# Kernel tuning notes

Measured on AMD Instinct MI355X. Metric: run time of the kernel, lower is better.

Reference implementation:

```python
import jax, jax.numpy as jnp
import numpy as np

EPS = 1e-05


def setup_inputs() -> dict:
    key = jax.random.key(0)
    ks = jax.random.split(key, 6)
    B, L, D = 16, 4096, 1024
    x = jax.random.normal(ks[0], (B, L, D), dtype=jnp.float32)
    prev_count = jax.random.randint(ks[1], (B,), 1, 5).astype(jnp.int32)  # prior_count-like, >=1
    prev_mean = jnp.zeros((B, D), dtype=jnp.float32)   # prior_mean init = 0
    prev_var = jnp.ones((B, D), dtype=jnp.float32)     # exp(prior_logv) with logv init 0
    weight = 0.02 * jax.random.normal(ks[2], (D,), dtype=jnp.float32)
    bias = 0.02 * jax.random.normal(ks[3], (D,), dtype=jnp.float32)
    padding_mask = jax.random.randint(ks[4], (B, L), 0, 2).astype(bool)  # True = padded
    return {"x": x, "prev_count": prev_count, "prev_mean": prev_mean,
            "prev_var": prev_var, "weight": weight, "bias": bias,
            "padding_mask": padding_mask}


def _timestep_norm(x, prev_count, prev_mean, prev_var, gamma, beta, padding_mask, eps):
    # x: [B, L, D]; Welford running mean/var over timesteps, skipping padded steps.
    B, L, D = x.shape
    valid = (~padding_mask).astype(x.dtype)          # [B, L], 1 = valid step
    x_t = jnp.swapaxes(x, 0, 1)                      # [L, B, D]
    m_t = valid.T                                    # [L, B]

    def step(carry, inp):
        count, mean, var = carry                     # [B], [B,D], [B,D]
        xt, m = inp                                  # [B,D], [B]
        mb = m[:, None]                              # [B,1]
        new_count = count + m                        # [B]
        denom = jnp.maximum(new_count, 1.0)[:, None]
        delta = xt - mean
        new_mean = mean + mb * delta / denom
        var_upd = (count[:, None] * var + delta * (xt - new_mean)) / denom
        new_var = jnp.where(mb > 0, var_upd, var)
        y = (gamma * (xt - new_mean) * jax.lax.rsqrt(new_var + eps) + beta) * mb
        return (new_count, new_mean, new_var), y

    init = (prev_count.astype(x.dtype), prev_mean, prev_var)
    (count, mean, var), ys = jax.lax.scan(step, init, (x_t, m_t))
    y = jnp.swapaxes(ys, 0, 1)                       # [B, L, D]
    return y, count, mean, var


def reference(x, prev_count, prev_mean, prev_var, weight, bias, padding_mask):
    gamma = weight + 1.0
    return _timestep_norm(x, prev_count, prev_mean, prev_var, gamma, bias,
                          padding_mask, EPS)
```

## Files before the change

### kernel.cpp

```cpp
#include <hip/hip_runtime.h>


#define Bn 16
#define Ln 4096
#define Dn 1024
#define D4 (Dn / 4)
#define Cn 128
#define CLn (Ln / Cn)
#define EPSf 1e-5f

struct St { float n; float4 m; float4 s; };

__device__ __forceinline__ St chan_merge(const St& A, const St& B) {
    St R;
    R.n = A.n + B.n;
    float wB = B.n / fmaxf(R.n, 1.f);
    float sc = A.n * wB;
    float dx = B.m.x - A.m.x, dy = B.m.y - A.m.y,
          dz = B.m.z - A.m.z, dw = B.m.w - A.m.w;
    R.m.x = A.m.x + dx * wB; R.m.y = A.m.y + dy * wB;
    R.m.z = A.m.z + dz * wB; R.m.w = A.m.w + dw * wB;
    R.s.x = A.s.x + B.s.x + dx * dx * sc; R.s.y = A.s.y + B.s.y + dy * dy * sc;
    R.s.z = A.s.z + B.s.z + dz * dz * sc; R.s.w = A.s.w + B.s.w + dw * dw * sc;
    return R;
}

__device__ __forceinline__ St shfl_up_st(const St& v, int delta) {
    St r;
    r.n   = __shfl_up(v.n,   delta, 64);
    r.m.x = __shfl_up(v.m.x, delta, 64); r.m.y = __shfl_up(v.m.y, delta, 64);
    r.m.z = __shfl_up(v.m.z, delta, 64); r.m.w = __shfl_up(v.m.w, delta, 64);
    r.s.x = __shfl_up(v.s.x, delta, 64); r.s.y = __shfl_up(v.s.y, delta, 64);
    r.s.z = __shfl_up(v.s.z, delta, 64); r.s.w = __shfl_up(v.s.w, delta, 64);
    return r;
}

__global__ __launch_bounds__(256) void tn_chunk_stats(
    const float* __restrict__ x, const int* __restrict__ mask,
    float4* __restrict__ mean_ws, float4* __restrict__ m2_ws,
    float* __restrict__ cnt_ws)
{
    int idx = blockIdx.x * 256 + threadIdx.x;
    int d4 = idx & (D4 - 1);
    int bc = idx >> 8;
    int c  = bc & (Cn - 1);
    int b  = bc >> 7;

    const float4* xp = (const float4*)(x + ((size_t)b * Ln + (size_t)c * CLn) * Dn) + d4;
    const int*    mp = mask + b * Ln + c * CLn;

    float n = 0.f;
    float4 mean = {0.f, 0.f, 0.f, 0.f};
    float4 M2   = {0.f, 0.f, 0.f, 0.f};
    #pragma unroll 8
    for (int i = 0; i < CLn; ++i) {
        float4 xv = xp[(size_t)i * D4];
        if (mp[i] == 0) {
            n += 1.f;
            float rn = 1.f / n;
            float dx;
            dx = xv.x - mean.x; mean.x += dx * rn; M2.x += dx * (xv.x - mean.x);
            dx = xv.y - mean.y; mean.y += dx * rn; M2.y += dx * (xv.y - mean.y);
            dx = xv.z - mean.z; mean.z += dx * rn; M2.z += dx * (xv.z - mean.z);
            dx = xv.w - mean.w; mean.w += dx * rn; M2.w += dx * (xv.w - mean.w);
        }
    }
    int o = (b * D4 + d4) * Cn + c;
    mean_ws[o] = mean;
    m2_ws[o]   = M2;
    if (d4 == 0) cnt_ws[bc] = n;
}

__global__ __launch_bounds__(256) void tn_scan(
    const int* __restrict__ prev_count, const float4* __restrict__ prev_mean,
    const float4* __restrict__ prev_var,
    float4* __restrict__ mean_ws, float4* __restrict__ m2_ws,
    const float* __restrict__ cnt_ws, float* __restrict__ cnt_pref,
    float* __restrict__ out_count, float4* __restrict__ out_mean,
    float4* __restrict__ out_var)
{
    int wv   = (blockIdx.x * 256 + threadIdx.x) >> 6;
    int lane = threadIdx.x & 63;
    int b  = wv >> 8;
    int d4 = wv & (D4 - 1);
    int base = (b * D4 + d4) * Cn;
    int c0 = 2 * lane, c1 = 2 * lane + 1;

    St s0, s1;
    s0.n = cnt_ws[b * Cn + c0]; s0.m = mean_ws[base + c0]; s0.s = m2_ws[base + c0];
    s1.n = cnt_ws[b * Cn + c1]; s1.m = mean_ws[base + c1]; s1.s = m2_ws[base + c1];

    St incl = chan_merge(s0, s1);
    #pragma unroll
    for (int off = 1; off < 64; off <<= 1) {
        St t = shfl_up_st(incl, off);
        if (lane >= off) incl = chan_merge(t, incl);
    }
    St epp = shfl_up_st(incl, 1);
    if (lane == 0) {
        epp.n = 0.f;
        epp.m = {0.f, 0.f, 0.f, 0.f};
        epp.s = {0.f, 0.f, 0.f, 0.f};
    }

    float np = (float)prev_count[b];
    St P;
    P.n = np;
    P.m = prev_mean[b * D4 + d4];
    float4 vp = prev_var[b * D4 + d4];
    P.s = {vp.x * np, vp.y * np, vp.z * np, vp.w * np};

    St pref0 = chan_merge(P, epp);
    St pref1 = chan_merge(pref0, s0);

    mean_ws[base + c0] = pref0.m; m2_ws[base + c0] = pref0.s;
    mean_ws[base + c1] = pref1.m; m2_ws[base + c1] = pref1.s;
    if (d4 == 0) {
        cnt_pref[b * Cn + c0] = pref0.n;
        cnt_pref[b * Cn + c1] = pref1.n;
    }

    if (lane == 63) {
        St tot = chan_merge(P, incl);
        out_mean[b * D4 + d4] = tot.m;
        float rn = 1.f / tot.n;
        out_var[b * D4 + d4] = {tot.s.x * rn, tot.s.y * rn, tot.s.z * rn, tot.s.w * rn};
        if (d4 == 0) out_count[b] = tot.n;
    }
}

__global__ __launch_bounds__(256) void tn_emit(
    const float* __restrict__ x, const int* __restrict__ mask,
    const float* __restrict__ weight, const float* __restrict__ bias,
    const float4* __restrict__ mean_ws, const float4* __restrict__ m2_ws,
    const float* __restrict__ cnt_pref, float* __restrict__ y)
{
    int idx = blockIdx.x * 256 + threadIdx.x;
    int d4 = idx & (D4 - 1);
    int bc = idx >> 8;
    int c  = bc & (Cn - 1);
    int b  = bc >> 7;

    size_t gbase = ((size_t)b * Ln + (size_t)c * CLn) * Dn;
    const float4* xp = (const float4*)(x + gbase) + d4;
    float4*       yp = (float4*)(y + gbase) + d4;
    const int*    mp = mask + b * Ln + c * CLn;

    int o = (b * D4 + d4) * Cn + c;
    float  n    = cnt_pref[bc];
    float4 mean = mean_ws[o];
    float4 M2   = m2_ws[o];
    const float4 w4 = ((const float4*)weight)[d4];
    const float4 b4 = ((const float4*)bias)[d4];
    float gx = w4.x + 1.f, gy = w4.y + 1.f, gz = w4.z + 1.f, gw = w4.w + 1.f;

    #pragma unroll 4
    for (int i = 0; i < CLn; ++i) {
        float4 yv = {0.f, 0.f, 0.f, 0.f};
        if (mp[i] == 0) {
            float4 xv = xp[(size_t)i * D4];
            n += 1.f;
            float rn = 1.f / n;
            float dx, d2;
            dx = xv.x - mean.x; mean.x += dx * rn; d2 = xv.x - mean.x;
            M2.x += dx * d2; yv.x = gx * d2 * rsqrtf(M2.x * rn + EPSf) + b4.x;
            dx = xv.y - mean.y; mean.y += dx * rn; d2 = xv.y - mean.y;
            M2.y += dx * d2; yv.y = gy * d2 * rsqrtf(M2.y * rn + EPSf) + b4.y;
            dx = xv.z - mean.z; mean.z += dx * rn; d2 = xv.z - mean.z;
            M2.z += dx * d2; yv.z = gz * d2 * rsqrtf(M2.z * rn + EPSf) + b4.z;
            dx = xv.w - mean.w; mean.w += dx * rn; d2 = xv.w - mean.w;
            M2.w += dx * d2; yv.w = gw * d2 * rsqrtf(M2.w * rn + EPSf) + b4.w;
        }
        yp[(size_t)i * D4] = yv;
    }
}

extern "C" void kernel_launch(void* const* d_in, const int* in_sizes, int n_in,
                              void* d_out, int out_size, void* d_ws, size_t ws_size,
                              hipStream_t stream)
{
    const float* x          = (const float*)d_in[0];
    const int*   prev_count = (const int*)d_in[1];
    const float* prev_mean  = (const float*)d_in[2];
    const float* prev_var   = (const float*)d_in[3];
    const float* weight     = (const float*)d_in[4];
    const float* bias       = (const float*)d_in[5];
    const int*   mask       = (const int*)d_in[6];

    float* y         = (float*)d_out;
    float* out_count = y + (size_t)Bn * Ln * Dn;
    float* out_mean  = out_count + Bn;
    float* out_var   = out_mean + (size_t)Bn * Dn;

    float4* mean_ws  = (float4*)d_ws;
    float4* m2_ws    = mean_ws + (size_t)Bn * D4 * Cn;
    float*  cnt_ws   = (float*)(m2_ws + (size_t)Bn * D4 * Cn);
    float*  cnt_pref = cnt_ws + Bn * Cn;

    tn_chunk_stats<<<(Bn * Cn * D4) / 256, 256, 0, stream>>>(
        x, mask, mean_ws, m2_ws, cnt_ws);
    tn_scan<<<(Bn * D4 * 64) / 256, 256, 0, stream>>>(
        prev_count, (const float4*)prev_mean, (const float4*)prev_var,
        mean_ws, m2_ws, cnt_ws, cnt_pref,
        out_count, (float4*)out_mean, (float4*)out_var);
    tn_emit<<<(Bn * Cn * D4) / 256, 256, 0, stream>>>(
        x, mask, weight, bias, mean_ws, m2_ws, cnt_pref, y);
}
```

Baseline: 503.9 us.

## Fuse chunk stats, scan and emit into single-pass decoupled look-back kernel

```diff
diff --git a/kernel.cpp b/kernel.cpp
--- a/kernel.cpp
+++ b/kernel.cpp
@@ -7,6 +7,7 @@
 #define D4 (Dn / 4)
 #define Cn 128
 #define CLn (Ln / Cn)
+#define NCH (Bn * Cn)
 #define EPSf 1e-5f
 
 struct St { float n; float4 m; float4 s; };
@@ -25,134 +26,117 @@
     return R;
 }
 
-__device__ __forceinline__ St shfl_up_st(const St& v, int delta) {
-    St r;
-    r.n   = __shfl_up(v.n,   delta, 64);
-    r.m.x = __shfl_up(v.m.x, delta, 64); r.m.y = __shfl_up(v.m.y, delta, 64);
-    r.m.z = __shfl_up(v.m.z, delta, 64); r.m.w = __shfl_up(v.m.w, delta, 64);
-    r.s.x = __shfl_up(v.s.x, delta, 64); r.s.y = __shfl_up(v.s.y, delta, 64);
-    r.s.z = __shfl_up(v.s.z, delta, 64); r.s.w = __shfl_up(v.s.w, delta, 64);
-    return r;
+__global__ __launch_bounds__(256) void tn_init(int* __restrict__ flags,
+                                               int* __restrict__ ticket)
+{
+    int i = threadIdx.x;
+    #pragma unroll
+    for (int k = 0; k < NCH / 256; ++k) flags[k * 256 + i] = 0;
+    if (i == 0) *ticket = 0;
 }
 
-__global__ __launch_bounds__(256) void tn_chunk_stats(
+__global__ __launch_bounds__(256) void tn_fused(
     const float* __restrict__ x, const int* __restrict__ mask,
-    float4* __restrict__ mean_ws, float4* __restrict__ m2_ws,
-    float* __restrict__ cnt_ws)
+    const int* __restrict__ prev_count, const float4* __restrict__ prev_mean,
+    const float4* __restrict__ prev_var,
+    const float* __restrict__ weight, const float* __restrict__ bias,
+    float4* __restrict__ agg_mean, float4* __restrict__ agg_m2,
+    float4* __restrict__ pref_mean, float4* __restrict__ pref_m2,
+    float* __restrict__ agg_n, float* __restrict__ pref_n,
+    int* __restrict__ flags, int* __restrict__ ticket,
+    float* __restrict__ y, float* __restrict__ out_count,
+    float4* __restrict__ out_mean, float4* __restrict__ out_var)
 {
-    int idx = blockIdx.x * 256 + threadIdx.x;
-    int d4 = idx & (D4 - 1);
-    int bc = idx >> 8;
-    int c  = bc & (Cn - 1);
-    int b  = bc >> 7;
+    __shared__ int s_vt, s_stop, s_mode;
+    if (threadIdx.x == 0) s_vt = atomicAdd(ticket, 1) & (NCH - 1);
+    __syncthreads();
+    int vt = s_vt;
+    int c  = vt >> 4;
+    int b  = vt & (Bn - 1);
+    int ch = b * Cn + c;
+    int d4 = threadIdx.x;
 
-    const float4* xp = (const float4*)(x + ((size_t)b * Ln + (size_t)c * CLn) * Dn) + d4;
+    size_t gbase = ((size_t)b * Ln + (size_t)c * CLn) * Dn;
+    const float4* xp = (const float4*)(x + gbase) + d4;
     const int*    mp = mask + b * Ln + c * CLn;
 
-    float n = 0.f;
-    float4 mean = {0.f, 0.f, 0.f, 0.f};
-    float4 M2   = {0.f, 0.f, 0.f, 0.f};
+    St A; A.n = 0.f; A.m = {0.f, 0.f, 0.f, 0.f}; A.s = {0.f, 0.f, 0.f, 0.f};
     #pragma unroll 8
     for (int i = 0; i < CLn; ++i) {
         float4 xv = xp[(size_t)i * D4];
         if (mp[i] == 0) {
-            n += 1.f;
-            float rn = 1.f / n;
+            A.n += 1.f;
+            float rn = 1.f / A.n;
             float dx;
-            dx = xv.x - mean.x; mean.x += dx * rn; M2.x += dx * (xv.x - mean.x);
-            dx = xv.y - mean.y; mean.y += dx * rn; M2.y += dx * (xv.y - mean.y);
-            dx = xv.z - mean.z; mean.z += dx * rn; M2.z += dx * (xv.z - mean.z);
-            dx = xv.w - mean.w; mean.w += dx * rn; M2.w += dx * (xv.w - mean.w);
+            dx = xv.x - A.m.x; A.m.x += dx * rn; A.s.x += dx * (xv.x - A.m.x);
+            dx = xv.y - A.m.y; A.m.y += dx * rn; A.s.y += dx * (xv.y - A.m.y);
+            dx = xv.z - A.m.z; A.m.z += dx * rn; A.s.z += dx * (xv.z - A.m.z);
+            dx = xv.w - A.m.w; A.m.w += dx * rn; A.s.w += dx * (xv.w - A.m.w);
         }
     }
-    int o = (b * D4 + d4) * Cn + c;
-    mean_ws[o] = mean;
-    m2_ws[o]   = M2;
-    if (d4 == 0) cnt_ws[bc] = n;
-}
 
-__global__ __launch_bounds__(256) void tn_scan(
-    const int* __restrict__ prev_count, const float4* __restrict__ prev_mean,
-    const float4* __restrict__ prev_var,
-    float4* __restrict__ mean_ws, float4* __restrict__ m2_ws,
-    const float* __restrict__ cnt_ws, float* __restrict__ cnt_pref,
-    float* __restrict__ out_count, float4* __restrict__ out_mean,
-    float4* __restrict__ out_var)
-{
-    int wv   = (blockIdx.x * 256 + threadIdx.x) >> 6;
-    int lane = threadIdx.x & 63;
-    int b  = wv >> 8;
-    int d4 = wv & (D4 - 1);
-    int base = (b * D4 + d4) * Cn;
-    int c0 = 2 * lane, c1 = 2 * lane + 1;
+    agg_mean[(size_t)ch * D4 + d4] = A.m;
+    agg_m2  [(size_t)ch * D4 + d4] = A.s;
+    if (threadIdx.x == 0) agg_n[ch] = A.n;
+    __threadfence();
+    __syncthreads();
+    if (threadIdx.x == 0) atomicExch(&flags[ch], 1);
 
-    St s0, s1;
-    s0.n = cnt_ws[b * Cn + c0]; s0.m = mean_ws[base + c0]; s0.s = m2_ws[base + c0];
-    s1.n = cnt_ws[b * Cn + c1]; s1.m = mean_ws[base + c1]; s1.s = m2_ws[base + c1];
+    if (threadIdx.x == 0) {
+        int look = c - 1, mode = 0;
+        while (look >= 0) {
+            int f = atomicAdd(&flags[b * Cn + look], 0);
+            if (f == 0) { __builtin_amdgcn_s_sleep(2); continue; }
+            if (f == 2) { mode = 1; break; }
+            --look;
+        }
+        s_stop = look; s_mode = mode;
+    }
+    __syncthreads();
+    __threadfence();
+    int stop = s_stop, mode = s_mode;
 
-    St incl = chan_merge(s0, s1);
-    #pragma unroll
-    for (int off = 1; off < 64; off <<= 1) {
-        St t = shfl_up_st(incl, off);
-        if (lane >= off) incl = chan_merge(t, incl);
+    St E;
+    if (mode == 1) {
+        E.n = pref_n[b * Cn + stop];
+        E.m = pref_mean[(size_t)(b * Cn + stop) * D4 + d4];
+        E.s = pref_m2  [(size_t)(b * Cn + stop) * D4 + d4];
+    } else {
+        E.n = (float)prev_count[b];
+        E.m = prev_mean[b * D4 + d4];
+        float4 vp = prev_var[b * D4 + d4];
+        E.s = {vp.x * E.n, vp.y * E.n, vp.z * E.n, vp.w * E.n};
     }
-    St epp = shfl_up_st(incl, 1);
-    if (lane == 0) {
-        epp.n = 0.f;
-        epp.m = {0.f, 0.f, 0.f, 0.f};
-        epp.s = {0.f, 0.f, 0.f, 0.f};
+    for (int l = stop + 1; l < c; ++l) {
+        St ag;
+        ag.n = agg_n[b * Cn + l];
+        ag.m = agg_mean[(size_t)(b * Cn + l) * D4 + d4];
+        ag.s = agg_m2  [(size_t)(b * Cn + l) * D4 + d4];
+        E = chan_merge(E, ag);
     }
 
-    float np = (float)prev_count[b];
-    St P;
-    P.n = np;
-    P.m = prev_mean[b * D4 + d4];
-    float4 vp = prev_var[b * D4 + d4];
-    P.s = {vp.x * np, vp.y * np, vp.z * np, vp.w * np};
+    St I = chan_merge(E, A);
+    pref_mean[(size_t)ch * D4 + d4] = I.m;
+    pref_m2  [(size_t)ch * D4 + d4] = I.s;
+    if (threadIdx.x == 0) pref_n[ch] = I.n;
+    __threadfence();
+    __syncthreads();
+    if (threadIdx.x == 0) atomicExch(&flags[ch], 2);
 
-    St pref0 = chan_merge(P, epp);
-    St pref1 = chan_merge(pref0, s0);
-
-    mean_ws[base + c0] = pref0.m; m2_ws[base + c0] = pref0.s;
-    mean_ws[base + c1] = pref1.m; m2_ws[base + c1] = pref1.s;
-    if (d4 == 0) {
-        cnt_pref[b * Cn + c0] = pref0.n;
-        cnt_pref[b * Cn + c1] = pref1.n;
+    if (c == Cn - 1) {
+        out_mean[b * D4 + d4] = I.m;
+        float rn = 1.f / I.n;
+        out_var[b * D4 + d4] = {I.s.x * rn, I.s.y * rn, I.s.z * rn, I.s.w * rn};
+        if (threadIdx.x == 0) out_count[b] = I.n;
     }
 
-    if (lane == 63) {
-        St tot = chan_merge(P, incl);
-        out_mean[b * D4 + d4] = tot.m;
-        float rn = 1.f / tot.n;
-        out_var[b * D4 + d4] = {tot.s.x * rn, tot.s.y * rn, tot.s.z * rn, tot.s.w * rn};
-        if (d4 == 0) out_count[b] = tot.n;
-    }
-}
-
-__global__ __launch_bounds__(256) void tn_emit(
-    const float* __restrict__ x, const int* __restrict__ mask,
-    const float* __restrict__ weight, const float* __restrict__ bias,
-    const float4* __restrict__ mean_ws, const float4* __restrict__ m2_ws,
-    const float* __restrict__ cnt_pref, float* __restrict__ y)
-{
-    int idx = blockIdx.x * 256 + threadIdx.x;
-    int d4 = idx & (D4 - 1);
-    int bc = idx >> 8;
-    int c  = bc & (Cn - 1);
-    int b  = bc >> 7;
-
-    size_t gbase = ((size_t)b * Ln + (size_t)c * CLn) * Dn;
-    const float4* xp = (const float4*)(x + gbase) + d4;
-    float4*       yp = (float4*)(y + gbase) + d4;
-    const int*    mp = mask + b * Ln + c * CLn;
-
-    int o = (b * D4 + d4) * Cn + c;
-    float  n    = cnt_pref[bc];
-    float4 mean = mean_ws[o];
-    float4 M2   = m2_ws[o];
     const float4 w4 = ((const float4*)weight)[d4];
     const float4 b4 = ((const float4*)bias)[d4];
     float gx = w4.x + 1.f, gy = w4.y + 1.f, gz = w4.z + 1.f, gw = w4.w + 1.f;
+    float  n    = E.n;
+    float4 mean = E.m;
+    float4 M2   = E.s;
+    float4* yp = (float4*)(y + gbase) + d4;
 
     #pragma unroll 4
     for (int i = 0; i < CLn; ++i) {
@@ -192,17 +176,19 @@
     float* out_mean  = out_count + Bn;
     float* out_var   = out_mean + (size_t)Bn * Dn;
 
-    float4* mean_ws  = (float4*)d_ws;
-    float4* m2_ws    = mean_ws + (size_t)Bn * D4 * Cn;
-    float*  cnt_ws   = (float*)(m2_ws + (size_t)Bn * D4 * Cn);
-    float*  cnt_pref = cnt_ws + Bn * Cn;
+    float4* agg_mean  = (float4*)d_ws;
+    float4* agg_m2    = agg_mean  + (size_t)NCH * D4;
+    float4* pref_mean = agg_m2    + (size_t)NCH * D4;
+    float4* pref_m2   = pref_mean + (size_t)NCH * D4;
+    float*  agg_n     = (float*)(pref_m2 + (size_t)NCH * D4);
+    float*  pref_n    = agg_n + NCH;
+    int*    flags     = (int*)(pref_n + NCH);
+    int*    ticket    = flags + NCH;
 
-    tn_chunk_stats<<<(Bn * Cn * D4) / 256, 256, 0, stream>>>(
-        x, mask, mean_ws, m2_ws, cnt_ws);
-    tn_scan<<<(Bn * D4 * 64) / 256, 256, 0, stream>>>(
-        prev_count, (const float4*)prev_mean, (const float4*)prev_var,
-        mean_ws, m2_ws, cnt_ws, cnt_pref,
-        out_count, (float4*)out_mean, (float4*)out_var);
-    tn_emit<<<(Bn * Cn * D4) / 256, 256, 0, stream>>>(
-        x, mask, weight, bias, mean_ws, m2_ws, cnt_pref, y);
+    tn_init<<<1, 256, 0, stream>>>(flags, ticket);
+    tn_fused<<<NCH, 256, 0, stream>>>(
+        x, mask, prev_count, (const float4*)prev_mean, (const float4*)prev_var,
+        weight, bias,
+        agg_mean, agg_m2, pref_mean, pref_m2, agg_n, pref_n, flags, ticket,
+        y, out_count, (float4*)out_mean, (float4*)out_var);
 }
```

Measured after the change: 1.437 ms. 2.85x slower.
